# Optimization experiments

Hardware: AMD Instinct MI355X
Metric: run time of the kernel (lower is better)

Reference implementation:

```python
import jax, jax.numpy as jnp
import numpy as np

NUM_JOINTS = 32
N_E = 1024
E_DIM = 128
BETA = 0.25
HID = 256
CHAINS = [[0,1,2,3,4,5],[0,6,7,8,9,10],[0,11,12,13,14,15],
          [12,16,17,18,19,20,21,22,23],[12,24,25,26,27,28,29,30,31]]


def setup_inputs() -> dict:
    key = jax.random.key(0)
    ks = jax.random.split(key, 8)
    B, T = 64, 128
    z = jax.random.normal(ks[0], (B, T, NUM_JOINTS, E_DIM), jnp.float32)
    # xavier_uniform for embeddings: bound = sqrt(6/(n_e+e_dim))
    eb = float(np.sqrt(6.0 / (N_E + E_DIM)))
    emb = jax.random.uniform(ks[1], (NUM_JOINTS, N_E, E_DIM), jnp.float32, -eb, eb)
    # torch Linear default init: U(-1/sqrt(fan_in), 1/sqrt(fan_in))
    b1b = float(1.0 / np.sqrt(2 * E_DIM))
    W1 = jax.random.uniform(ks[2], (2 * E_DIM, HID), jnp.float32, -b1b, b1b)
    b1 = jax.random.uniform(ks[3], (HID,), jnp.float32, -b1b, b1b)
    ln_g = jnp.ones((HID,), jnp.float32)
    ln_b = jnp.zeros((HID,), jnp.float32)
    b2b = float(1.0 / np.sqrt(HID))
    W2 = jax.random.uniform(ks[4], (HID, E_DIM), jnp.float32, -b2b, b2b)
    b2 = jax.random.uniform(ks[5], (E_DIM,), jnp.float32, -b2b, b2b)
    return {"z": z, "emb": emb, "W1": W1, "b1": b1, "ln_g": ln_g,
            "ln_b": ln_b, "W2": W2, "b2": b2}


def _layernorm(x, g, b, eps=1e-5):
    m = jnp.mean(x, axis=-1, keepdims=True)
    v = jnp.mean((x - m) ** 2, axis=-1, keepdims=True)
    return (x - m) * jax.lax.rsqrt(v + eps) * g + b


def _mlp(x, W1, b1, ln_g, ln_b, W2, b2):
    h = x @ W1 + b1
    h = jax.nn.relu(_layernorm(h, ln_g, ln_b))
    return h @ W2 + b2


def _quantize_joint(h, E):
    # h: [B,T,C], E: [n_e,C]. argmin of euclidean dist == argmin of -2 h.E^T + |E|^2
    B, T, C = h.shape
    hf = h.reshape(-1, C)
    d = -2.0 * (hf @ E.T) + jnp.sum(E * E, axis=1)  # [B*T, n_e]
    idx = jnp.argmin(d, axis=1)
    e = E[idx].reshape(B, T, C)  # one-hot @ E == gather
    sg = jax.lax.stop_gradient
    loss = jnp.mean((sg(e) - h) ** 2) + BETA * jnp.mean((e - sg(h)) ** 2)
    q = h + sg(e - h)  # straight-through
    return q, e, idx.reshape(B, T), loss


def reference(z, emb, W1, b1, ln_g, ln_b, W2, b2):
    B, T, V, C = z.shape
    sg = jax.lax.stop_gradient
    stored_q, stored_e, stored_idx = {}, {}, {}
    total = jnp.zeros((), z.dtype)
    for chain in CHAINS:
        parent_e = None
        for i, j in enumerate(chain):
            if j not in stored_q:  # single-pass per joint
                zj = z[:, :, j, :]
                h = _mlp(jnp.concatenate([parent_e, zj], -1), W1, b1, ln_g, ln_b, W2, b2) if i > 0 else zj
                q, e, idx, loss = _quantize_joint(h, emb[j])
                stored_q[j], stored_e[j], stored_idx[j] = q, e, idx
                total = total + loss
            parent_e = sg(stored_e[j])
    z_q = jnp.stack([stored_q[v] for v in range(V)], axis=2)      # [B,T,V,C]
    indices = jnp.stack([stored_idx[v] for v in range(V)], axis=2)  # [B,T,V]
    return z_q, total / V, indices
```

## Files before the change

kernel.cpp:

```cpp
#include <hip/hip_runtime.h>

#define NJ 32
#define NE 1024
#define CD 128
#define HID 256
#define ROWS 8192

struct Lv { int nj; int j[5]; int p[5]; };

typedef __attribute__((ext_vector_type(2))) float f2;

#define PKLO(acc, s0, s1) \
  asm("v_pk_fma_f32 %0, %1, %2, %0 op_sel:[0,0,0] op_sel_hi:[0,1,1]" \
      : "+v"(acc) : "v"(s0), "v"(s1))
#define PKHI(acc, s0, s1) \
  asm("v_pk_fma_f32 %0, %1, %2, %0 op_sel:[1,0,0] op_sel_hi:[1,1,1]" \
      : "+v"(acc) : "v"(s0), "v"(s1))

__global__ __launch_bounds__(256) void norms_kernel(const float* __restrict__ emb,
                                                    float* __restrict__ nrm) {
  int gid = blockIdx.x * 256 + threadIdx.x;
  int n = gid >> 2, l = gid & 3;
  const float* row = emb + (size_t)n * CD;
  float s = 0.f;
#pragma unroll
  for (int i = 0; i < 8; ++i) {
    float4 v = *(const float4*)&row[(l + 4 * i) * 4];
    s += v.x * v.x + v.y * v.y + v.z * v.z + v.w * v.w;
  }
  s += __shfl_xor(s, 1);
  s += __shfl_xor(s, 2);
  if (l == 0) nrm[n] = s;
}

template <int RB>
__global__ __launch_bounds__(256) void fused_level(
    const float* __restrict__ z, const float* __restrict__ emb,
    const float* __restrict__ W1, const float* __restrict__ b1,
    const float* __restrict__ lng, const float* __restrict__ lnb,
    const float* __restrict__ W2, const float* __restrict__ b2,
    const float* __restrict__ nrm,
    float* __restrict__ zq, float* __restrict__ idx_out,
    float* __restrict__ partials, Lv lv, int pbase) {
  constexpr int RPG = RB / 8;
  constexpr int R4 = RB / 4;
  constexpr int HSP = RB + 4;
  constexpr int BPJ = ROWS / RB;
  constexpr int XS_SZ = 32 * HSP;
  constexpr int HS_SZ = 128 * HSP;
  constexpr int P1 = XS_SZ + 8448;
  constexpr int P3 = HS_SZ + 2112;
  constexpr int P4 = HS_SZ + 16 * 516 + 512;
  constexpr int SM12 = (P1 > P3) ? P1 : P3;
  constexpr int SMEM = (SM12 > P4) ? SM12 : P4;

  __shared__ __align__(16) float smem[SMEM];
  __shared__ float wsum[4];
  float* xs  = smem;
  float* ws1 = smem + XS_SZ;
  float* as_ = smem;
  float* ws2 = smem + HS_SZ;
  float* hs  = smem;
  float* es  = smem + HS_SZ;
  float* nsm = smem + HS_SZ + 16 * 516;

  const int tid = threadIdx.x;
  const int rg = tid >> 5, cg = tid & 31;
  const int u = cg & 15;
  const int qcA = (cg >> 4) * 128 + u * 4;
  const int qcB = qcA + 64;
  const int jl = blockIdx.x / BPJ;
  const int row0 = (blockIdx.x % BPJ) * RB;
  const int jj = lv.j[jl], pj = lv.p[jl];
  const size_t rstride = (size_t)NJ * CD;

  if (pj >= 0) {
    f2 acc1[RPG][4];
#pragma unroll
    for (int r = 0; r < RPG; ++r)
#pragma unroll
      for (int c = 0; c < 4; ++c) acc1[r][c] = (f2){0.f, 0.f};

#pragma unroll 1
    for (int ks = 0; ks < 8; ++ks) {
#pragma unroll
      for (int uu = 0; uu < RB / 32; ++uu) {
        int idx = uu * 256 + tid;
        int r = idx >> 3, kq = idx & 7;
        const float* src = (ks < 4)
            ? (zq + (size_t)(row0 + r) * rstride + (size_t)pj * CD + (ks * 32 + kq * 4))
            : (z  + (size_t)(row0 + r) * rstride + (size_t)jj * CD + (ks * 32 - 128 + kq * 4));
        float4 v = *(const float4*)src;
        xs[(kq * 4 + 0) * HSP + r] = v.x;
        xs[(kq * 4 + 1) * HSP + r] = v.y;
        xs[(kq * 4 + 2) * HSP + r] = v.z;
        xs[(kq * 4 + 3) * HSP + r] = v.w;
      }
#pragma unroll
      for (int v8 = 0; v8 < 8; ++v8) {
        int idx = v8 * 256 + tid;
        int k = idx >> 6, c4 = idx & 63;
        *(float4*)&ws1[k * 264 + c4 * 4] =
            *(const float4*)&W1[(size_t)(ks * 32 + k) * HID + c4 * 4];
      }
      __syncthreads();
#pragma unroll 2
      for (int kk = 0; kk < 32; ++kk) {
        f2 xrp[RPG / 2], wcp[4];
#pragma unroll
        for (int g = 0; g < RPG / 4; ++g)
          *(float4*)&xrp[g * 2] = *(const float4*)&xs[kk * HSP + rg * RPG + g * 4];
        *(float4*)&wcp[0] = *(const float4*)&ws1[kk * 264 + qcA];
        *(float4*)&wcp[2] = *(const float4*)&ws1[kk * 264 + qcB];
#pragma unroll
        for (int r2 = 0; r2 < RPG / 2; ++r2) {
#pragma unroll
          for (int c = 0; c < 4; ++c) PKLO(acc1[2 * r2][c], xrp[r2], wcp[c]);
#pragma unroll
          for (int c = 0; c < 4; ++c) PKHI(acc1[2 * r2 + 1][c], xrp[r2], wcp[c]);
        }
      }
      __syncthreads();
    }

    {
      float bb[8], gg[8], be[8];
      *(float4*)&bb[0] = *(const float4*)&b1[qcA];
      *(float4*)&bb[4] = *(const float4*)&b1[qcB];
      *(float4*)&gg[0] = *(const float4*)&lng[qcA];
      *(float4*)&gg[4] = *(const float4*)&lng[qcB];
      *(float4*)&be[0] = *(const float4*)&lnb[qcA];
      *(float4*)&be[4] = *(const float4*)&lnb[qcB];
#pragma unroll
      for (int r = 0; r < RPG; ++r) {
        float s0 = 0.f, q0 = 0.f;
#pragma unroll
        for (int j = 0; j < 8; ++j) {
          float v = acc1[r][j >> 1][j & 1] + bb[j];
          acc1[r][j >> 1][j & 1] = v;
          s0 += v; q0 += v * v;
        }
        float si = __shfl_xor(s0, 16), qi = __shfl_xor(q0, 16);
        float s1 = si, q1 = qi;
#pragma unroll
        for (int j = 0; j < 8; ++j) {
          float v = acc1[r][j >> 1][j & 1];
          s1 += v; q1 += v * v;
        }
#pragma unroll
        for (int m = 1; m < 16; m <<= 1) {
          s1 += __shfl_xor(s1, m); q1 += __shfl_xor(q1, m);
        }
        float s2 = __shfl_xor(s1, 16), q2 = __shfl_xor(q1, 16);
        float Sx = (cg & 16) ? s1 : s2;
        float Qx = (cg & 16) ? q1 : q2;
        float mu = Sx * (1.f / HID);
        float va = Qx * (1.f / HID) - mu * mu;
        float iv = 1.f / sqrtf(va + 1e-5f);
#pragma unroll
        for (int j = 0; j < 8; ++j) {
          float a = (acc1[r][j >> 1][j & 1] - mu) * iv * gg[j] + be[j];
          acc1[r][j >> 1][j & 1] = fmaxf(a, 0.f);
        }
      }
    }

    f2 acc2[RPG][2];
#pragma unroll
    for (int r = 0; r < RPG; ++r)
#pragma unroll
      for (int c = 0; c < 2; ++c) acc2[r][c] = (f2){0.f, 0.f};

#pragma unroll 1
    for (int half = 0; half < 2; ++half) {
      __syncthreads();
      if ((cg >> 4) == half) {
#pragma unroll
        for (int j = 0; j < 8; ++j) {
          int kl = (j >> 2) * 64 + u * 4 + (j & 3);
#pragma unroll
          for (int g = 0; g < RPG; ++g)
            as_[kl * HSP + rg * RPG + g] = acc1[g][j >> 1][j & 1];
        }
      }
      __syncthreads();
#pragma unroll 1
      for (int kc = 0; kc < 8; ++kc) {
#pragma unroll
        for (int v = 0; v < 2; ++v) {
          int idx = v * 256 + tid;
          int k = idx >> 5, c4 = idx & 31;
          *(float4*)&ws2[k * 132 + c4 * 4] =
              *(const float4*)&W2[(size_t)(half * 128 + kc * 16 + k) * CD + c4 * 4];
        }
        __syncthreads();
#pragma unroll 2
        for (int kk = 0; kk < 16; ++kk) {
          f2 arp[RPG / 2], w2p[2];
#pragma unroll
          for (int g = 0; g < RPG / 4; ++g)
            *(float4*)&arp[g * 2] =
                *(const float4*)&as_[(kc * 16 + kk) * HSP + rg * RPG + g * 4];
          *(float4*)&w2p[0] = *(const float4*)&ws2[kk * 132 + cg * 4];
#pragma unroll
          for (int r2 = 0; r2 < RPG / 2; ++r2) {
#pragma unroll
            for (int c = 0; c < 2; ++c) PKLO(acc2[2 * r2][c], arp[r2], w2p[c]);
#pragma unroll
            for (int c = 0; c < 2; ++c) PKHI(acc2[2 * r2 + 1][c], arp[r2], w2p[c]);
          }
        }
        __syncthreads();
      }
    }
    {
      float4 bv = *(const float4*)&b2[cg * 4];
      float bb2[4] = {bv.x, bv.y, bv.z, bv.w};
#pragma unroll
      for (int c = 0; c < 4; ++c) {
#pragma unroll
        for (int g = 0; g < RPG / 4; ++g)
          *(float4*)&hs[(cg * 4 + c) * HSP + rg * RPG + g * 4] =
              make_float4(acc2[g * 4 + 0][c >> 1][c & 1] + bb2[c],
                          acc2[g * 4 + 1][c >> 1][c & 1] + bb2[c],
                          acc2[g * 4 + 2][c >> 1][c & 1] + bb2[c],
                          acc2[g * 4 + 3][c >> 1][c & 1] + bb2[c]);
      }
    }
  } else {
#pragma unroll
    for (int v = 0; v < RB / 8; ++v) {
      int idx = v * 256 + tid;
      int r = idx >> 5, c4 = idx & 31;
      float4 vz = *(const float4*)&z[(size_t)(row0 + r) * rstride + (size_t)jj * CD + c4 * 4];
      hs[(c4 * 4 + 0) * HSP + r] = vz.x;
      hs[(c4 * 4 + 1) * HSP + r] = vz.y;
      hs[(c4 * 4 + 2) * HSP + r] = vz.z;
      hs[(c4 * 4 + 3) * HSP + r] = vz.w;
    }
  }

  const int w4 = tid >> 6;
  const int l4 = tid & 63;
  float mnv[R4]; int mni[R4];
#pragma unroll
  for (int r = 0; r < R4; ++r) { mnv[r] = 3.402823e38f; mni[r] = 0; }
  const float* embJ = emb + (size_t)jj * NE * CD;
  const float* nrmJ = nrm + jj * NE;

#pragma unroll 1
  for (int p = 0; p < 2; ++p) {
    __syncthreads();
    if (tid < 128) {
      *(float4*)&nsm[tid * 4] = *(const float4*)&nrmJ[p * 512 + tid * 4];
    }
    f2 acc4[R4][4];
#pragma unroll
    for (int r = 0; r < R4; ++r)
#pragma unroll
      for (int c = 0; c < 4; ++c) acc4[r][c] = (f2){0.f, 0.f};

#pragma unroll 1
    for (int kc = 0; kc < 8; ++kc) {
#pragma unroll
      for (int v = 0; v < 8; ++v) {
        int idx = v * 256 + tid;
        int n = idx >> 2, kq = idx & 3;
        float4 ev = *(const float4*)&embJ[(size_t)(p * 512 + n) * CD + kc * 16 + kq * 4];
        es[(kq * 4 + 0) * 516 + n] = ev.x;
        es[(kq * 4 + 1) * 516 + n] = ev.y;
        es[(kq * 4 + 2) * 516 + n] = ev.z;
        es[(kq * 4 + 3) * 516 + n] = ev.w;
      }
      __syncthreads();
#pragma unroll 2
      for (int kk = 0; kk < 16; ++kk) {
        int c = kc * 16 + kk;
        f2 hrp[R4 / 2], ecp[4];
#pragma unroll
        for (int g = 0; g < R4 / 4; ++g)
          *(float4*)&hrp[g * 2] = *(const float4*)&hs[c * HSP + w4 * R4 + g * 4];
        *(float4*)&ecp[0] = *(const float4*)&es[kk * 516 + l4 * 4];
        *(float4*)&ecp[2] = *(const float4*)&es[kk * 516 + 256 + l4 * 4];
#pragma unroll
        for (int r2 = 0; r2 < R4 / 2; ++r2) {
#pragma unroll
          for (int c2 = 0; c2 < 4; ++c2) PKLO(acc4[2 * r2][c2], hrp[r2], ecp[c2]);
#pragma unroll
          for (int c2 = 0; c2 < 4; ++c2) PKHI(acc4[2 * r2 + 1][c2], hrp[r2], ecp[c2]);
        }
      }
      __syncthreads();
    }
#pragma unroll
    for (int r = 0; r < R4; ++r) {
#pragma unroll
      for (int q = 0; q < 2; ++q) {
#pragma unroll
        for (int j = 0; j < 4; ++j) {
          int nl = q * 256 + l4 * 4 + j;
          int ci = q * 4 + j;
          float d = nsm[nl] - 2.f * acc4[r][ci >> 1][ci & 1];
          int n = p * 512 + nl;
          if (d < mnv[r]) { mnv[r] = d; mni[r] = n; }
        }
      }
    }
  }

#pragma unroll
  for (int r = 0; r < R4; ++r) {
    float mv = mnv[r]; int mi = mni[r];
#pragma unroll
    for (int m = 1; m < 64; m <<= 1) {
      float om = __shfl_xor(mv, m); int oi = __shfl_xor(mi, m);
      if (om < mv || (om == mv && oi < mi)) { mv = om; mi = oi; }
    }
    mnv[r] = mv; mni[r] = mi;
  }

  float lsum = 0.f;
#pragma unroll
  for (int r = 0; r < R4; ++r) {
    int row = w4 * R4 + r;
    int id = mni[r];
    const float* erow = embJ + (size_t)id * CD;
    float2 ev = *(const float2*)&erow[l4 * 2];
    float h0 = hs[(l4 * 2 + 0) * HSP + row];
    float h1 = hs[(l4 * 2 + 1) * HSP + row];
    float dx = ev.x - h0, dy = ev.y - h1;
    lsum += dx * dx + dy * dy;
    *(float2*)&zq[(size_t)(row0 + row) * rstride + (size_t)jj * CD + l4 * 2] = ev;
    if (l4 == r) idx_out[(size_t)(row0 + row) * NJ + jj] = (float)id;
  }
#pragma unroll
  for (int m = 1; m < 64; m <<= 1) lsum += __shfl_xor(lsum, m);
  if (l4 == 0) wsum[w4] = lsum;
  __syncthreads();
  if (tid == 0) partials[pbase + blockIdx.x] = wsum[0] + wsum[1] + wsum[2] + wsum[3];
}

__global__ __launch_bounds__(256) void loss_reduce(const float* __restrict__ p, int n,
                                                   float* __restrict__ out) {
  __shared__ float ws[4];
  float s = 0.f;
  for (int i = threadIdx.x; i < n; i += 256) s += p[i];
#pragma unroll
  for (int m = 1; m < 64; m <<= 1) s += __shfl_xor(s, m);
  if ((threadIdx.x & 63) == 0) ws[threadIdx.x >> 6] = s;
  __syncthreads();
  if (threadIdx.x == 0)
    out[0] = (ws[0] + ws[1] + ws[2] + ws[3]) * (1.25f / (1048576.f * 32.f));
}

extern "C" void kernel_launch(void* const* d_in, const int* in_sizes, int n_in,
                              void* d_out, int out_size, void* d_ws, size_t ws_size,
                              hipStream_t stream) {
  const float* z = (const float*)d_in[0];
  const float* emb = (const float*)d_in[1];
  const float* W1 = (const float*)d_in[2];
  const float* b1 = (const float*)d_in[3];
  const float* lng = (const float*)d_in[4];
  const float* lnb = (const float*)d_in[5];
  const float* W2 = (const float*)d_in[6];
  const float* b2 = (const float*)d_in[7];

  float* zq = (float*)d_out;
  float* loss = zq + (size_t)ROWS * NJ * CD;
  float* idxo = loss + 1;

  float* nrm = (float*)d_ws;
  float* partials = nrm + NJ * NE;

  norms_kernel<<<NJ * NE * 4 / 256, 256, 0, stream>>>(emb, nrm);

  static const Lv levels[11] = {
      {1, {0, 0, 0, 0, 0}, {-1, 0, 0, 0, 0}},
      {3, {1, 6, 11, 0, 0}, {0, 0, 0, 0, 0}},
      {3, {2, 7, 12, 0, 0}, {1, 6, 11, 0, 0}},
      {5, {3, 8, 13, 16, 24}, {2, 7, 12, 12, 12}},
      {5, {4, 9, 14, 17, 25}, {3, 8, 13, 16, 24}},
      {5, {5, 10, 15, 18, 26}, {4, 9, 14, 17, 25}},
      {2, {19, 27, 0, 0, 0}, {18, 26, 0, 0, 0}},
      {2, {20, 28, 0, 0, 0}, {19, 27, 0, 0, 0}},
      {2, {21, 29, 0, 0, 0}, {20, 28, 0, 0, 0}},
      {2, {22, 30, 0, 0, 0}, {21, 29, 0, 0, 0}},
      {2, {23, 31, 0, 0, 0}, {22, 30, 0, 0, 0}},
  };
  static const int rbs[11] = {16, 64, 64, 64, 64, 64, 32, 32, 32, 32, 32};

  int pbase = 0;
  for (int L = 0; L < 11; ++L) {
    int bpj = ROWS / rbs[L];
    int blocks = levels[L].nj * bpj;
    if (rbs[L] == 64) {
      fused_level<64><<<blocks, 256, 0, stream>>>(
          z, emb, W1, b1, lng, lnb, W2, b2, nrm, zq, idxo, partials, levels[L], pbase);
    } else if (rbs[L] == 32) {
      fused_level<32><<<blocks, 256, 0, stream>>>(
          z, emb, W1, b1, lng, lnb, W2, b2, nrm, zq, idxo, partials, levels[L], pbase);
    } else {
      fused_level<16><<<blocks, 256, 0, stream>>>(
          z, emb, W1, b1, lng, lnb, W2, b2, nrm, zq, idxo, partials, levels[L], pbase);
    }
    pbase += blocks;
  }
  loss_reduce<<<1, 256, 0, stream>>>(partials, pbase, loss);
}
```

Before: 1.834 ms.

## Spill transposed h to global scratch and read it as wave-uniform scalar loads

For the RB=64 levels, each block writes its transposed h tile to a global workspace buffer. In the codebook distance loop it then reads the 16 row values per wave through a wave-uniform pointer (readfirstlane), so they can become scalar loads instead of LDS reads. The packed FMA asm is replaced by plain scalar FMAs that use those uniform operands. This cuts LDS bandwidth pressure in the hot loop, at the cost of extra global writes and reads and a dependency on workspace size, with a fallback to the old path when the workspace is too small.

```diff
diff --git a/kernel.cpp b/kernel.cpp
--- a/kernel.cpp
+++ b/kernel.cpp
@@ -9,6 +9,7 @@
 struct Lv { int nj; int j[5]; int p[5]; };
 
 typedef __attribute__((ext_vector_type(2))) float f2;
+typedef __attribute__((ext_vector_type(16))) float f16v;
 
 #define PKLO(acc, s0, s1) \
   asm("v_pk_fma_f32 %0, %1, %2, %0 op_sel:[0,0,0] op_sel_hi:[0,1,1]" \
@@ -33,13 +34,13 @@
   if (l == 0) nrm[n] = s;
 }
 
-template <int RB>
+template <int RB, int HT>
 __global__ __launch_bounds__(256) void fused_level(
     const float* __restrict__ z, const float* __restrict__ emb,
     const float* __restrict__ W1, const float* __restrict__ b1,
     const float* __restrict__ lng, const float* __restrict__ lnb,
     const float* __restrict__ W2, const float* __restrict__ b2,
-    const float* __restrict__ nrm,
+    const float* __restrict__ nrm, float* __restrict__ hT,
     float* __restrict__ zq, float* __restrict__ idx_out,
     float* __restrict__ partials, Lv lv, int pbase) {
   constexpr int RPG = RB / 8;
@@ -73,6 +74,8 @@
   const int row0 = (blockIdx.x % BPJ) * RB;
   const int jj = lv.j[jl], pj = lv.p[jl];
   const size_t rstride = (size_t)NJ * CD;
+  float* hTblk = HT ? (hT + (size_t)(jl * BPJ + (blockIdx.x % BPJ)) * (64 * 128))
+                    : nullptr;
 
   if (pj >= 0) {
     f2 acc1[RPG][4];
@@ -219,12 +222,15 @@
 #pragma unroll
       for (int c = 0; c < 4; ++c) {
 #pragma unroll
-        for (int g = 0; g < RPG / 4; ++g)
-          *(float4*)&hs[(cg * 4 + c) * HSP + rg * RPG + g * 4] =
-              make_float4(acc2[g * 4 + 0][c >> 1][c & 1] + bb2[c],
-                          acc2[g * 4 + 1][c >> 1][c & 1] + bb2[c],
-                          acc2[g * 4 + 2][c >> 1][c & 1] + bb2[c],
-                          acc2[g * 4 + 3][c >> 1][c & 1] + bb2[c]);
+        for (int g = 0; g < RPG / 4; ++g) {
+          float4 hv4 = make_float4(acc2[g * 4 + 0][c >> 1][c & 1] + bb2[c],
+                                   acc2[g * 4 + 1][c >> 1][c & 1] + bb2[c],
+                                   acc2[g * 4 + 2][c >> 1][c & 1] + bb2[c],
+                                   acc2[g * 4 + 3][c >> 1][c & 1] + bb2[c]);
+          *(float4*)&hs[(cg * 4 + c) * HSP + rg * RPG + g * 4] = hv4;
+          if constexpr (HT)
+            *(float4*)&hTblk[(cg * 4 + c) * 64 + rg * RPG + g * 4] = hv4;
+        }
       }
     }
   } else {
@@ -237,6 +243,12 @@
       hs[(c4 * 4 + 1) * HSP + r] = vz.y;
       hs[(c4 * 4 + 2) * HSP + r] = vz.z;
       hs[(c4 * 4 + 3) * HSP + r] = vz.w;
+      if constexpr (HT) {
+        hTblk[(c4 * 4 + 0) * 64 + r] = vz.x;
+        hTblk[(c4 * 4 + 1) * 64 + r] = vz.y;
+        hTblk[(c4 * 4 + 2) * 64 + r] = vz.z;
+        hTblk[(c4 * 4 + 3) * 64 + r] = vz.w;
+      }
     }
   }
 
@@ -248,61 +260,120 @@
   const float* embJ = emb + (size_t)jj * NE * CD;
   const float* nrmJ = nrm + jj * NE;
 
-#pragma unroll 1
-  for (int p = 0; p < 2; ++p) {
-    __syncthreads();
-    if (tid < 128) {
-      *(float4*)&nsm[tid * 4] = *(const float4*)&nrmJ[p * 512 + tid * 4];
-    }
-    f2 acc4[R4][4];
-#pragma unroll
-    for (int r = 0; r < R4; ++r)
-#pragma unroll
-      for (int c = 0; c < 4; ++c) acc4[r][c] = (f2){0.f, 0.f};
-
-#pragma unroll 1
-    for (int kc = 0; kc < 8; ++kc) {
-#pragma unroll
-      for (int v = 0; v < 8; ++v) {
-        int idx = v * 256 + tid;
-        int n = idx >> 2, kq = idx & 3;
-        float4 ev = *(const float4*)&embJ[(size_t)(p * 512 + n) * CD + kc * 16 + kq * 4];
-        es[(kq * 4 + 0) * 516 + n] = ev.x;
-        es[(kq * 4 + 1) * 516 + n] = ev.y;
-        es[(kq * 4 + 2) * 516 + n] = ev.z;
-        es[(kq * 4 + 3) * 516 + n] = ev.w;
-      }
-      __syncthreads();
+  if constexpr (HT) {
+    const int w4u = __builtin_amdgcn_readfirstlane(w4);
+    const float* hTw = hTblk + w4u * 16;
+#pragma unroll 1
+    for (int p = 0; p < 2; ++p) {
+      __syncthreads();
+      if (tid < 128) {
+        *(float4*)&nsm[tid * 4] = *(const float4*)&nrmJ[p * 512 + tid * 4];
+      }
+      float acc4[R4][8];
+#pragma unroll
+      for (int r = 0; r < R4; ++r)
+#pragma unroll
+        for (int c = 0; c < 8; ++c) acc4[r][c] = 0.f;
+
+#pragma unroll 1
+      for (int kc = 0; kc < 8; ++kc) {
+#pragma unroll
+        for (int v = 0; v < 8; ++v) {
+          int idx = v * 256 + tid;
+          int n = idx >> 2, kq = idx & 3;
+          float4 ev = *(const float4*)&embJ[(size_t)(p * 512 + n) * CD + kc * 16 + kq * 4];
+          es[(kq * 4 + 0) * 516 + n] = ev.x;
+          es[(kq * 4 + 1) * 516 + n] = ev.y;
+          es[(kq * 4 + 2) * 516 + n] = ev.z;
+          es[(kq * 4 + 3) * 516 + n] = ev.w;
+        }
+        __syncthreads();
 #pragma unroll 2
-      for (int kk = 0; kk < 16; ++kk) {
-        int c = kc * 16 + kk;
-        f2 hrp[R4 / 2], ecp[4];
-#pragma unroll
-        for (int g = 0; g < R4 / 4; ++g)
-          *(float4*)&hrp[g * 2] = *(const float4*)&hs[c * HSP + w4 * R4 + g * 4];
-        *(float4*)&ecp[0] = *(const float4*)&es[kk * 516 + l4 * 4];
-        *(float4*)&ecp[2] = *(const float4*)&es[kk * 516 + 256 + l4 * 4];
-#pragma unroll
-        for (int r2 = 0; r2 < R4 / 2; ++r2) {
-#pragma unroll
-          for (int c2 = 0; c2 < 4; ++c2) PKLO(acc4[2 * r2][c2], hrp[r2], ecp[c2]);
-#pragma unroll
-          for (int c2 = 0; c2 < 4; ++c2) PKHI(acc4[2 * r2 + 1][c2], hrp[r2], ecp[c2]);
-        }
-      }
-      __syncthreads();
-    }
-#pragma unroll
-    for (int r = 0; r < R4; ++r) {
-#pragma unroll
-      for (int q = 0; q < 2; ++q) {
-#pragma unroll
-        for (int j = 0; j < 4; ++j) {
-          int nl = q * 256 + l4 * 4 + j;
-          int ci = q * 4 + j;
-          float d = nsm[nl] - 2.f * acc4[r][ci >> 1][ci & 1];
-          int n = p * 512 + nl;
-          if (d < mnv[r]) { mnv[r] = d; mni[r] = n; }
+        for (int kk = 0; kk < 16; ++kk) {
+          int c = kc * 16 + kk;
+          f16v hv = *(const f16v*)(hTw + c * 64);
+          float ec[8];
+          *(float4*)&ec[0] = *(const float4*)&es[kk * 516 + l4 * 4];
+          *(float4*)&ec[4] = *(const float4*)&es[kk * 516 + 256 + l4 * 4];
+#pragma unroll
+          for (int r = 0; r < R4; ++r)
+#pragma unroll
+            for (int c2 = 0; c2 < 8; ++c2)
+              acc4[r][c2] += hv[r] * ec[c2];
+        }
+        __syncthreads();
+      }
+#pragma unroll
+      for (int r = 0; r < R4; ++r) {
+#pragma unroll
+        for (int q = 0; q < 2; ++q) {
+#pragma unroll
+          for (int j = 0; j < 4; ++j) {
+            int nl = q * 256 + l4 * 4 + j;
+            float d = nsm[nl] - 2.f * acc4[r][q * 4 + j];
+            int n = p * 512 + nl;
+            if (d < mnv[r]) { mnv[r] = d; mni[r] = n; }
+          }
+        }
+      }
+    }
+  } else {
+#pragma unroll 1
+    for (int p = 0; p < 2; ++p) {
+      __syncthreads();
+      if (tid < 128) {
+        *(float4*)&nsm[tid * 4] = *(const float4*)&nrmJ[p * 512 + tid * 4];
+      }
+      f2 acc4[R4][4];
+#pragma unroll
+      for (int r = 0; r < R4; ++r)
+#pragma unroll
+        for (int c = 0; c < 4; ++c) acc4[r][c] = (f2){0.f, 0.f};
+
+#pragma unroll 1
+      for (int kc = 0; kc < 8; ++kc) {
+#pragma unroll
+        for (int v = 0; v < 8; ++v) {
+          int idx = v * 256 + tid;
+          int n = idx >> 2, kq = idx & 3;
+          float4 ev = *(const float4*)&embJ[(size_t)(p * 512 + n) * CD + kc * 16 + kq * 4];
+          es[(kq * 4 + 0) * 516 + n] = ev.x;
+          es[(kq * 4 + 1) * 516 + n] = ev.y;
+          es[(kq * 4 + 2) * 516 + n] = ev.z;
+          es[(kq * 4 + 3) * 516 + n] = ev.w;
+        }
+        __syncthreads();
+#pragma unroll 2
+        for (int kk = 0; kk < 16; ++kk) {
+          int c = kc * 16 + kk;
+          f2 hrp[R4 / 2], ecp[4];
+#pragma unroll
+          for (int g = 0; g < R4 / 4; ++g)
+            *(float4*)&hrp[g * 2] = *(const float4*)&hs[c * HSP + w4 * R4 + g * 4];
+          *(float4*)&ecp[0] = *(const float4*)&es[kk * 516 + l4 * 4];
+          *(float4*)&ecp[2] = *(const float4*)&es[kk * 516 + 256 + l4 * 4];
+#pragma unroll
+          for (int r2 = 0; r2 < R4 / 2; ++r2) {
+#pragma unroll
+            for (int c2 = 0; c2 < 4; ++c2) PKLO(acc4[2 * r2][c2], hrp[r2], ecp[c2]);
+#pragma unroll
+            for (int c2 = 0; c2 < 4; ++c2) PKHI(acc4[2 * r2 + 1][c2], hrp[r2], ecp[c2]);
+          }
+        }
+        __syncthreads();
+      }
+#pragma unroll
+      for (int r = 0; r < R4; ++r) {
+#pragma unroll
+        for (int q = 0; q < 2; ++q) {
+#pragma unroll
+          for (int j = 0; j < 4; ++j) {
+            int nl = q * 256 + l4 * 4 + j;
+            int ci = q * 4 + j;
+            float d = nsm[nl] - 2.f * acc4[r][ci >> 1][ci & 1];
+            int n = p * 512 + nl;
+            if (d < mnv[r]) { mnv[r] = d; mni[r] = n; }
+          }
         }
       }
     }
@@ -371,6 +442,10 @@
 
   float* nrm = (float*)d_ws;
   float* partials = nrm + NJ * NE;
+  float* hT = (float*)((char*)d_ws + 163840);
+
+  const size_t NEEDED = 163840 + (size_t)640 * 64 * 128 * 4;
+  const bool use_ht = (ws_size >= NEEDED);
 
   norms_kernel<<<NJ * NE * 4 / 256, 256, 0, stream>>>(emb, nrm);
 
@@ -394,14 +469,23 @@
     int bpj = ROWS / rbs[L];
     int blocks = levels[L].nj * bpj;
     if (rbs[L] == 64) {
-      fused_level<64><<<blocks, 256, 0, stream>>>(
-          z, emb, W1, b1, lng, lnb, W2, b2, nrm, zq, idxo, partials, levels[L], pbase);
+      if (use_ht) {
+        fused_level<64, 1><<<blocks, 256, 0, stream>>>(
+            z, emb, W1, b1, lng, lnb, W2, b2, nrm, hT, zq, idxo, partials,
+            levels[L], pbase);
+      } else {
+        fused_level<64, 0><<<blocks, 256, 0, stream>>>(
+            z, emb, W1, b1, lng, lnb, W2, b2, nrm, hT, zq, idxo, partials,
+            levels[L], pbase);
+      }
     } else if (rbs[L] == 32) {
-      fused_level<32><<<blocks, 256, 0, stream>>>(
-          z, emb, W1, b1, lng, lnb, W2, b2, nrm, zq, idxo, partials, levels[L], pbase);
+      fused_level<32, 0><<<blocks, 256, 0, stream>>>(
+          z, emb, W1, b1, lng, lnb, W2, b2, nrm, hT, zq, idxo, partials,
+          levels[L], pbase);
     } else {
-      fused_level<16><<<blocks, 256, 0, stream>>>(
-          z, emb, W1, b1, lng, lnb, W2, b2, nrm, zq, idxo, partials, levels[L], pbase);
+      fused_level<16, 0><<<blocks, 256, 0, stream>>>(
+          z, emb, W1, b1, lng, lnb, W2, b2, nrm, hT, zq, idxo, partials,
+          levels[L], pbase);
     }
     pbase += blocks;
   }
```

Result: slower. 1.962 ms (+6.9%).
